# Optimization experiments

Hardware: AMD Instinct MI355X
Metric: run time of the kernel (lower is better)

## Reference

```python
import jax, jax.numpy as jnp
import numpy as np

HIDDEN = 512
NUM_HEAD = 8
HEAD_DIM = HIDDEN // NUM_HEAD


def setup_inputs() -> dict:
    key = jax.random.key(0)
    ks = jax.random.split(key, 12)
    B, S = 8, 1024
    inp = {
        "v": jax.random.normal(ks[0], (B, S, HIDDEN), dtype=jnp.float32),
        "k": jax.random.normal(ks[1], (B, S, HIDDEN), dtype=jnp.float32),
        "q": jax.random.normal(ks[2], (B, S, HIDDEN), dtype=jnp.float32),
        "mask": jnp.zeros((B, 1, 1, S), dtype=bool),
    }
    scale = 1.0 / np.sqrt(HIDDEN)
    inp["Wv"] = jax.random.normal(ks[3], (HIDDEN, HIDDEN), dtype=jnp.float32) * scale
    inp["bv"] = jax.random.normal(ks[4], (HIDDEN,), dtype=jnp.float32) * scale
    inp["Wk"] = jax.random.normal(ks[5], (HIDDEN, HIDDEN), dtype=jnp.float32) * scale
    inp["bk"] = jax.random.normal(ks[6], (HIDDEN,), dtype=jnp.float32) * scale
    inp["Wq"] = jax.random.normal(ks[7], (HIDDEN, HIDDEN), dtype=jnp.float32) * scale
    inp["bq"] = jax.random.normal(ks[8], (HIDDEN,), dtype=jnp.float32) * scale
    inp["Wm"] = jax.random.normal(ks[9], (HIDDEN, HIDDEN), dtype=jnp.float32) * scale
    inp["bm"] = jax.random.normal(ks[10], (HIDDEN,), dtype=jnp.float32) * scale
    return inp


def _split_heads(x):
    # [B, S, H*D] -> [B, H, S, D]
    B, S, _ = x.shape
    return x.reshape(B, S, NUM_HEAD, HEAD_DIM).transpose(0, 2, 1, 3)


def reference(v, k, q, mask, Wv, bv, Wk, bk, Wq, bq, Wm, bm):
    B, S, _ = q.shape
    # linear projections (torch Linear: x @ W.T + b)
    vh = _split_heads(v @ Wv.T + bv)
    kh = _split_heads(k @ Wk.T + bk)
    qh = _split_heads(q @ Wq.T + bq)
    scale = 1.0 / jnp.sqrt(jnp.asarray(HEAD_DIM, dtype=qh.dtype))
    scores = jnp.einsum('bhqd,bhkd->bhqk', qh, kh) * scale
    scores = jnp.where(mask, jnp.asarray(-10000.0, dtype=scores.dtype), scores)
    att_map = jax.nn.softmax(scores, axis=-1)
    atted = jnp.einsum('bhqk,bhkd->bhqd', att_map, vh)
    atted = atted.transpose(0, 2, 1, 3).reshape(B, S, HIDDEN)
    atted = atted @ Wm.T + bm
    return atted, att_map
```

## Files before the change

### kernel.cpp

```cpp
#include <hip/hip_runtime.h>
#include <cstddef>

#define SEQ 1024
#define HID 512
#define NH 8
#define HD 64

typedef __attribute__((ext_vector_type(8))) short bf16x8;
typedef __attribute__((ext_vector_type(4))) float f32x4;

__device__ inline unsigned short f2bf(float f) {
  unsigned u = __builtin_bit_cast(unsigned, f);
  return (unsigned short)((u + 0x7fffu + ((u >> 16) & 1u)) >> 16);
}

__global__ __launch_bounds__(256) void proj_qkv(
    const float* __restrict__ x0, const float* __restrict__ x1, const float* __restrict__ x2,
    const float* __restrict__ w0, const float* __restrict__ w1, const float* __restrict__ w2,
    const float* __restrict__ b0, const float* __restrict__ b1, const float* __restrict__ b2,
    unsigned short* __restrict__ o0, unsigned short* __restrict__ o1,
    unsigned short* __restrict__ o2) {
  __shared__ short As[128 * 64];
  __shared__ short Bs[128 * 64];

  const int z = blockIdx.z;
  const float* X = z == 0 ? x0 : (z == 1 ? x1 : x2);
  const float* W = z == 0 ? w0 : (z == 1 ? w1 : w2);
  const float* bias = z == 0 ? b0 : (z == 1 ? b1 : b2);
  unsigned short* out = z == 0 ? o0 : (z == 1 ? o1 : o2);
  const float scale = z == 0 ? 0.125f : 1.0f;

  const int t = threadIdx.x;
  const int lane = t & 63, wid = t >> 6;
  const int lg = lane >> 4, lr = lane & 15;
  const int wm = (wid >> 1) * 64, wn = (wid & 1) * 64;
  const int m0 = blockIdx.y * 128, n0 = blockIdx.x * 128;

  f32x4 acc[4][4];
  const f32x4 zf = {0.f, 0.f, 0.f, 0.f};
#pragma unroll
  for (int mg = 0; mg < 4; ++mg)
#pragma unroll
    for (int ng = 0; ng < 4; ++ng) acc[mg][ng] = zf;

  for (int k0 = 0; k0 < 512; k0 += 64) {
    __syncthreads();
#pragma unroll
    for (int i = 0; i < 4; ++i) {
      const int gi = t + i * 256;
      const int r = gi >> 3, g = gi & 7;
      const int dst = r * 64 + ((g ^ (r & 7)) * 8);
      {
        const float* src = X + (size_t)(m0 + r) * 512 + k0 + g * 8;
        const float4 a = *reinterpret_cast<const float4*>(src);
        const float4 b2 = *reinterpret_cast<const float4*>(src + 4);
        union { bf16x8 v; unsigned short u[8]; } p;
        p.u[0] = f2bf(a.x);  p.u[1] = f2bf(a.y);  p.u[2] = f2bf(a.z);  p.u[3] = f2bf(a.w);
        p.u[4] = f2bf(b2.x); p.u[5] = f2bf(b2.y); p.u[6] = f2bf(b2.z); p.u[7] = f2bf(b2.w);
        *reinterpret_cast<bf16x8*>(As + dst) = p.v;
      }
      {
        const float* srcw = W + (size_t)(n0 + r) * 512 + k0 + g * 8;
        const float4 wa = *reinterpret_cast<const float4*>(srcw);
        const float4 wb = *reinterpret_cast<const float4*>(srcw + 4);
        union { bf16x8 v; unsigned short u[8]; } q;
        q.u[0] = f2bf(wa.x); q.u[1] = f2bf(wa.y); q.u[2] = f2bf(wa.z); q.u[3] = f2bf(wa.w);
        q.u[4] = f2bf(wb.x); q.u[5] = f2bf(wb.y); q.u[6] = f2bf(wb.z); q.u[7] = f2bf(wb.w);
        *reinterpret_cast<bf16x8*>(Bs + dst) = q.v;
      }
    }
    __syncthreads();

#pragma unroll
    for (int c = 0; c < 2; ++c) {
      bf16x8 af[4], bfr[4];
#pragma unroll
      for (int mg = 0; mg < 4; ++mg) {
        const int r = wm + mg * 16 + lr;
        af[mg] = *reinterpret_cast<const bf16x8*>(As + r * 64 + (((lg + 4 * c) ^ (r & 7)) * 8));
      }
#pragma unroll
      for (int ng = 0; ng < 4; ++ng) {
        const int r = wn + ng * 16 + lr;
        bfr[ng] = *reinterpret_cast<const bf16x8*>(Bs + r * 64 + (((lg + 4 * c) ^ (r & 7)) * 8));
      }
#pragma unroll
      for (int mg = 0; mg < 4; ++mg)
#pragma unroll
        for (int ng = 0; ng < 4; ++ng)
          acc[mg][ng] =
              __builtin_amdgcn_mfma_f32_16x16x32_bf16(af[mg], bfr[ng], acc[mg][ng], 0, 0, 0);
    }
  }

  float bv[4];
#pragma unroll
  for (int ng = 0; ng < 4; ++ng) bv[ng] = bias[n0 + wn + ng * 16 + lr];

#pragma unroll
  for (int mg = 0; mg < 4; ++mg) {
#pragma unroll
    for (int reg = 0; reg < 4; ++reg) {
      const int m = m0 + wm + mg * 16 + 4 * lg + reg;
#pragma unroll
      for (int ng = 0; ng < 4; ++ng) {
        const int n = n0 + wn + ng * 16 + lr;
        const float cval = (acc[mg][ng][reg] + bv[ng]) * scale;
        const int b = m >> 10, s = m & 1023, h = n >> 6, d = n & 63;
        if (z == 2)
          out[(((size_t)(b * NH + h)) * HD + d) * SEQ + s] = f2bf(cval);
        else
          out[(((size_t)(b * NH + h)) * SEQ + s) * HD + d] = f2bf(cval);
      }
    }
  }
}

__global__ __launch_bounds__(256) void proj_out(const unsigned short* __restrict__ Xb,
                                                const float* __restrict__ W,
                                                const float* __restrict__ bias,
                                                float* __restrict__ outv) {
  __shared__ short As[128 * 64];
  __shared__ short Bs[128 * 64];

  const int t = threadIdx.x;
  const int lane = t & 63, wid = t >> 6;
  const int lg = lane >> 4, lr = lane & 15;
  const int wm = (wid >> 1) * 64, wn = (wid & 1) * 64;
  const int m0 = blockIdx.y * 128, n0 = blockIdx.x * 128;

  f32x4 acc[4][4];
  const f32x4 zf = {0.f, 0.f, 0.f, 0.f};
#pragma unroll
  for (int mg = 0; mg < 4; ++mg)
#pragma unroll
    for (int ng = 0; ng < 4; ++ng) acc[mg][ng] = zf;

  for (int k0 = 0; k0 < 512; k0 += 64) {
    __syncthreads();
#pragma unroll
    for (int i = 0; i < 4; ++i) {
      const int gi = t + i * 256;
      const int r = gi >> 3, g = gi & 7;
      const int dst = r * 64 + ((g ^ (r & 7)) * 8);
      *reinterpret_cast<bf16x8*>(As + dst) =
          *reinterpret_cast<const bf16x8*>(Xb + (size_t)(m0 + r) * 512 + k0 + g * 8);
      const float* srcw = W + (size_t)(n0 + r) * 512 + k0 + g * 8;
      const float4 wa = *reinterpret_cast<const float4*>(srcw);
      const float4 wb = *reinterpret_cast<const float4*>(srcw + 4);
      union { bf16x8 v; unsigned short u[8]; } q;
      q.u[0] = f2bf(wa.x); q.u[1] = f2bf(wa.y); q.u[2] = f2bf(wa.z); q.u[3] = f2bf(wa.w);
      q.u[4] = f2bf(wb.x); q.u[5] = f2bf(wb.y); q.u[6] = f2bf(wb.z); q.u[7] = f2bf(wb.w);
      *reinterpret_cast<bf16x8*>(Bs + dst) = q.v;
    }
    __syncthreads();

#pragma unroll
    for (int c = 0; c < 2; ++c) {
      bf16x8 af[4], bfr[4];
#pragma unroll
      for (int mg = 0; mg < 4; ++mg) {
        const int r = wm + mg * 16 + lr;
        af[mg] = *reinterpret_cast<const bf16x8*>(As + r * 64 + (((lg + 4 * c) ^ (r & 7)) * 8));
      }
#pragma unroll
      for (int ng = 0; ng < 4; ++ng) {
        const int r = wn + ng * 16 + lr;
        bfr[ng] = *reinterpret_cast<const bf16x8*>(Bs + r * 64 + (((lg + 4 * c) ^ (r & 7)) * 8));
      }
#pragma unroll
      for (int mg = 0; mg < 4; ++mg)
#pragma unroll
        for (int ng = 0; ng < 4; ++ng)
          acc[mg][ng] =
              __builtin_amdgcn_mfma_f32_16x16x32_bf16(af[mg], bfr[ng], acc[mg][ng], 0, 0, 0);
    }
  }

  float bv[4];
#pragma unroll
  for (int ng = 0; ng < 4; ++ng) bv[ng] = bias[n0 + wn + ng * 16 + lr];

#pragma unroll
  for (int mg = 0; mg < 4; ++mg) {
#pragma unroll
    for (int reg = 0; reg < 4; ++reg) {
      const int m = m0 + wm + mg * 16 + 4 * lg + reg;
#pragma unroll
      for (int ng = 0; ng < 4; ++ng) {
        const int n = n0 + wn + ng * 16 + lr;
        __builtin_nontemporal_store(acc[mg][ng][reg] + bv[ng], outv + (size_t)m * 512 + n);
      }
    }
  }
}

__global__ __launch_bounds__(256) void attn_mfma(const unsigned short* __restrict__ qh,
                                                 const unsigned short* __restrict__ kh,
                                                 const unsigned short* __restrict__ vhT,
                                                 const unsigned char* __restrict__ mask,
                                                 float* __restrict__ att_map,
                                                 unsigned short* __restrict__ atted) {
  __shared__ short Ks[128 * 64];
  __shared__ short Vt[64 * 128];
  __shared__ short Pw4[4][2048];
  __shared__ float maskf[1024];

  const int t = threadIdx.x;
  const int lane = t & 63, wid = t >> 6;
  const int lg = lane >> 4, lr = lane & 15;
  const int qt = blockIdx.x & 15;
  const int bh = blockIdx.x >> 4;
  const int b = bh >> 3, h = bh & 7;
  const int q0 = qt * 64 + wid * 16;

  const unsigned short* Qb = qh + ((size_t)bh * SEQ + q0) * HD;
  const unsigned short* Kb = kh + (size_t)bh * SEQ * HD;
  const unsigned short* Vb = vhT + (size_t)bh * HD * SEQ;
  const unsigned char* mrow = mask + (size_t)b * SEQ;

#pragma unroll
  for (int i = 0; i < 4; ++i) {
    const int idx = t + i * 256;
    maskf[idx] = mrow[idx] ? -10000.f : 0.f;
  }

  bf16x8 qf[2];
#pragma unroll
  for (int c = 0; c < 2; ++c)
    qf[c] = *reinterpret_cast<const bf16x8*>(Qb + (size_t)lr * HD + lg * 8 + 32 * c);

  const f32x4 zf = {0.f, 0.f, 0.f, 0.f};

  float rs = 0.f;
  for (int kt = 0; kt < 8; ++kt) {
    __syncthreads();
#pragma unroll
    for (int i = 0; i < 4; ++i) {
      const int gi = t + i * 256;
      const int r = gi >> 3, g = gi & 7;
      *reinterpret_cast<bf16x8*>(Ks + r * 64 + ((g ^ (r & 7)) * 8)) =
          *reinterpret_cast<const bf16x8*>(Kb + (size_t)(kt * 128 + r) * HD + g * 8);
    }
    __syncthreads();
#pragma unroll
    for (int cg = 0; cg < 8; ++cg) {
      f32x4 s = zf;
#pragma unroll
      for (int c = 0; c < 2; ++c) {
        const int r = cg * 16 + lr;
        const bf16x8 kf =
            *reinterpret_cast<const bf16x8*>(Ks + r * 64 + (((lg + 4 * c) ^ (r & 7)) * 8));
        s = __builtin_amdgcn_mfma_f32_16x16x32_bf16(kf, qf[c], s, 0, 0, 0);
      }
      const float4 madd =
          *reinterpret_cast<const float4*>(maskf + kt * 128 + cg * 16 + 4 * lg);
      rs += (__expf(s[0] + madd.x) + __expf(s[1] + madd.y)) +
            (__expf(s[2] + madd.z) + __expf(s[3] + madd.w));
    }
  }
  rs += __shfl_xor(rs, 16);
  rs += __shfl_xor(rs, 32);
  const float inv = 1.f / rs;

  f32x4 oacc[4] = {zf, zf, zf, zf};
  short* Pw = Pw4[wid];
  float* arow = att_map + ((size_t)bh * SEQ + q0 + lr) * SEQ + 4 * lg;

  for (int kt = 0; kt < 8; ++kt) {
    __syncthreads();
#pragma unroll
    for (int i = 0; i < 4; ++i) {
      {
        const int gi = t + i * 256;
        const int r = gi >> 3, g = gi & 7;
        *reinterpret_cast<bf16x8*>(Ks + r * 64 + ((g ^ (r & 7)) * 8)) =
            *reinterpret_cast<const bf16x8*>(Kb + (size_t)(kt * 128 + r) * HD + g * 8);
      }
      {
        const int gi = t + i * 256;
        const int d = gi >> 4, g = gi & 15;
        const int slot = (g & 8) | ((g & 7) ^ (d & 7));
        *reinterpret_cast<bf16x8*>(Vt + d * 128 + slot * 8) =
            *reinterpret_cast<const bf16x8*>(Vb + (size_t)d * SEQ + kt * 128 + g * 8);
      }
    }
    __syncthreads();

#pragma unroll
    for (int cg = 0; cg < 8; ++cg) {
      f32x4 s = zf;
#pragma unroll
      for (int c = 0; c < 2; ++c) {
        const int r = cg * 16 + lr;
        const bf16x8 kf =
            *reinterpret_cast<const bf16x8*>(Ks + r * 64 + (((lg + 4 * c) ^ (r & 7)) * 8));
        s = __builtin_amdgcn_mfma_f32_16x16x32_bf16(kf, qf[c], s, 0, 0, 0);
      }
      const float4 madd =
          *reinterpret_cast<const float4*>(maskf + kt * 128 + cg * 16 + 4 * lg);
      const float p0 = __expf(s[0] + madd.x);
      const float p1 = __expf(s[1] + madd.y);
      const float p2 = __expf(s[2] + madd.z);
      const float p3 = __expf(s[3] + madd.w);
      f32x4 w;
      w.x = p0 * inv; w.y = p1 * inv; w.z = p2 * inv; w.w = p3 * inv;
      __builtin_nontemporal_store(
          w, reinterpret_cast<f32x4*>(arow + kt * 128 + cg * 16));
      uint2 pr;
      pr.x = (unsigned)f2bf(p0) | ((unsigned)f2bf(p1) << 16);
      pr.y = (unsigned)f2bf(p2) | ((unsigned)f2bf(p3) << 16);
      const int gk = 2 * cg + (lg >> 1);
      *reinterpret_cast<uint2*>(Pw + lr * 128 + ((gk ^ (lr & 7)) * 8) + (lg & 1) * 4) = pr;
    }

#pragma unroll
    for (int c = 0; c < 4; ++c) {
      const bf16x8 pa =
          *reinterpret_cast<const bf16x8*>(Pw + lr * 128 + (((lg + 4 * c) ^ (lr & 7)) * 8));
#pragma unroll
      for (int ng = 0; ng < 4; ++ng) {
        const int d = ng * 16 + lr;
        const int gidx = 4 * c + lg;
        const int slot = (gidx & 8) | ((gidx & 7) ^ (d & 7));
        const bf16x8 vf = *reinterpret_cast<const bf16x8*>(Vt + d * 128 + slot * 8);
        oacc[ng] = __builtin_amdgcn_mfma_f32_16x16x32_bf16(pa, vf, oacc[ng], 0, 0, 0);
      }
    }
  }

  float invq[4];
#pragma unroll
  for (int reg = 0; reg < 4; ++reg) invq[reg] = __shfl(inv, 4 * lg + reg);
#pragma unroll
  for (int ng = 0; ng < 4; ++ng) {
#pragma unroll
    for (int reg = 0; reg < 4; ++reg) {
      const int q = q0 + 4 * lg + reg;
      const int d = ng * 16 + lr;
      atted[((size_t)b * SEQ + q) * HID + h * HD + d] = f2bf(oacc[ng][reg] * invq[reg]);
    }
  }
}

extern "C" void kernel_launch(void* const* d_in, const int* in_sizes, int n_in,
                              void* d_out, int out_size, void* d_ws, size_t ws_size,
                              hipStream_t stream) {
  const float* v = (const float*)d_in[0];
  const float* k = (const float*)d_in[1];
  const float* q = (const float*)d_in[2];
  const unsigned char* mask = (const unsigned char*)d_in[3];
  const float* Wv = (const float*)d_in[4];
  const float* bv = (const float*)d_in[5];
  const float* Wk = (const float*)d_in[6];
  const float* bk = (const float*)d_in[7];
  const float* Wq = (const float*)d_in[8];
  const float* bq = (const float*)d_in[9];
  const float* Wm = (const float*)d_in[10];
  const float* bm = (const float*)d_in[11];

  float* out_atted = (float*)d_out;
  float* out_att = out_atted + (size_t)8 * SEQ * HID;

  const size_t TN = (size_t)8 * SEQ * HID;
  unsigned short* qh = (unsigned short*)d_ws;
  unsigned short* kh = qh + TN;
  unsigned short* vhT = kh + TN;
  unsigned short* aw = vhT + TN;

  proj_qkv<<<dim3(4, 64, 3), 256, 0, stream>>>(q, k, v, Wq, Wk, Wv, bq, bk, bv, qh, kh, vhT);

  attn_mfma<<<dim3(1024), 256, 0, stream>>>(qh, kh, vhT, mask, out_att, aw);

  proj_out<<<dim3(4, 64), 256, 0, stream>>>(aw, Wm, bm, out_atted);
}
```

Baseline: 211.7 us.

## Read K and V fragments directly from global memory instead of LDS staging

Measured after the change: 254.1 us. +20.1%, slower.

```diff
diff --git a/kernel.cpp b/kernel.cpp
--- a/kernel.cpp
+++ b/kernel.cpp
@@ -195,14 +195,12 @@
   }
 }
 
-__global__ __launch_bounds__(256) void attn_mfma(const unsigned short* __restrict__ qh,
-                                                 const unsigned short* __restrict__ kh,
-                                                 const unsigned short* __restrict__ vhT,
-                                                 const unsigned char* __restrict__ mask,
-                                                 float* __restrict__ att_map,
-                                                 unsigned short* __restrict__ atted) {
-  __shared__ short Ks[128 * 64];
-  __shared__ short Vt[64 * 128];
+__global__ __launch_bounds__(256, 3) void attn_mfma(const unsigned short* __restrict__ qh,
+                                                    const unsigned short* __restrict__ kh,
+                                                    const unsigned short* __restrict__ vhT,
+                                                    const unsigned char* __restrict__ mask,
+                                                    float* __restrict__ att_map,
+                                                    unsigned short* __restrict__ atted) {
   __shared__ short Pw4[4][2048];
   __shared__ float maskf[1024];
 
@@ -224,6 +222,7 @@
     const int idx = t + i * 256;
     maskf[idx] = mrow[idx] ? -10000.f : 0.f;
   }
+  __syncthreads();
 
   bf16x8 qf[2];
 #pragma unroll
@@ -234,23 +233,14 @@
 
   float rs = 0.f;
   for (int kt = 0; kt < 8; ++kt) {
-    __syncthreads();
-#pragma unroll
-    for (int i = 0; i < 4; ++i) {
-      const int gi = t + i * 256;
-      const int r = gi >> 3, g = gi & 7;
-      *reinterpret_cast<bf16x8*>(Ks + r * 64 + ((g ^ (r & 7)) * 8)) =
-          *reinterpret_cast<const bf16x8*>(Kb + (size_t)(kt * 128 + r) * HD + g * 8);
-    }
-    __syncthreads();
 #pragma unroll
     for (int cg = 0; cg < 8; ++cg) {
+      const int r = kt * 128 + cg * 16 + lr;
       f32x4 s = zf;
 #pragma unroll
       for (int c = 0; c < 2; ++c) {
-        const int r = cg * 16 + lr;
         const bf16x8 kf =
-            *reinterpret_cast<const bf16x8*>(Ks + r * 64 + (((lg + 4 * c) ^ (r & 7)) * 8));
+            *reinterpret_cast<const bf16x8*>(Kb + (size_t)r * HD + (lg + 4 * c) * 8);
         s = __builtin_amdgcn_mfma_f32_16x16x32_bf16(kf, qf[c], s, 0, 0, 0);
       }
       const float4 madd =
@@ -268,33 +258,14 @@
   float* arow = att_map + ((size_t)bh * SEQ + q0 + lr) * SEQ + 4 * lg;
 
   for (int kt = 0; kt < 8; ++kt) {
-    __syncthreads();
-#pragma unroll
-    for (int i = 0; i < 4; ++i) {
-      {
-        const int gi = t + i * 256;
-        const int r = gi >> 3, g = gi & 7;
-        *reinterpret_cast<bf16x8*>(Ks + r * 64 + ((g ^ (r & 7)) * 8)) =
-            *reinterpret_cast<const bf16x8*>(Kb + (size_t)(kt * 128 + r) * HD + g * 8);
-      }
-      {
-        const int gi = t + i * 256;
-        const int d = gi >> 4, g = gi & 15;
-        const int slot = (g & 8) | ((g & 7) ^ (d & 7));
-        *reinterpret_cast<bf16x8*>(Vt + d * 128 + slot * 8) =
-            *reinterpret_cast<const bf16x8*>(Vb + (size_t)d * SEQ + kt * 128 + g * 8);
-      }
-    }
-    __syncthreads();
-
 #pragma unroll
     for (int cg = 0; cg < 8; ++cg) {
+      const int r = kt * 128 + cg * 16 + lr;
       f32x4 s = zf;
 #pragma unroll
       for (int c = 0; c < 2; ++c) {
-        const int r = cg * 16 + lr;
         const bf16x8 kf =
-            *reinterpret_cast<const bf16x8*>(Ks + r * 64 + (((lg + 4 * c) ^ (r & 7)) * 8));
+            *reinterpret_cast<const bf16x8*>(Kb + (size_t)r * HD + (lg + 4 * c) * 8);
         s = __builtin_amdgcn_mfma_f32_16x16x32_bf16(kf, qf[c], s, 0, 0, 0);
       }
       const float4 madd =
@@ -321,9 +292,8 @@
 #pragma unroll
       for (int ng = 0; ng < 4; ++ng) {
         const int d = ng * 16 + lr;
-        const int gidx = 4 * c + lg;
-        const int slot = (gidx & 8) | ((gidx & 7) ^ (d & 7));
-        const bf16x8 vf = *reinterpret_cast<const bf16x8*>(Vt + d * 128 + slot * 8);
+        const bf16x8 vf = *reinterpret_cast<const bf16x8*>(
+            Vb + (size_t)d * SEQ + kt * 128 + (4 * c + lg) * 8);
         oacc[ng] = __builtin_amdgcn_mfma_f32_16x16x32_bf16(pa, vf, oacc[ng], 0, 0, 0);
       }
     }
```
